# Kernel tuning notes

Hardware: AMD Instinct MI355X
Metric: run time of the kernel (lower is better)

The kernel has to match this reference:

```python
import jax, jax.numpy as jnp
import numpy as np


def _norm_group(pts, ref):
    # pts: [B,T,N,2], ref: [B,T,1,2]. Subtract reference point, divide both coords
    # by max(width,height) of the relative bbox (per frame), guarding scale==0.
    rel = pts - ref
    w = rel[..., 0].max(axis=-1) - rel[..., 0].min(axis=-1)
    h = rel[..., 1].max(axis=-1) - rel[..., 1].min(axis=-1)
    s = jnp.maximum(w, h)
    s = jnp.where(s == 0, jnp.ones_like(s), s)
    return rel / s[..., None, None]


def _prepare_input(x):
    B, T, _ = x.shape
    pts = x.reshape(B, T, 133, 2)
    left = _norm_group(pts[:, :, 91:112], pts[:, :, 9:10]).reshape(B, T, 42)
    right = _norm_group(pts[:, :, 112:133], pts[:, :, 10:11]).reshape(B, T, 42)
    center = pts[:, :, 0:1]
    left_arm = _norm_group(pts[:, :, (5, 7, 9), :], center).reshape(B, T, 6)
    right_arm = _norm_group(pts[:, :, (6, 8, 10), :], center).reshape(B, T, 6)
    return right, right_arm, left, left_arm


def _lstm(x, wih, whh, bih, bhh):
    # x: [B,T,F]; PyTorch gate order i,f,g,o. Returns all hidden states [B,T,H].
    B = x.shape[0]
    H = whh.shape[1]
    pre = jnp.einsum('btf,gf->btg', x, wih) + bih  # [B,T,4H]
    pre = pre.transpose(1, 0, 2)  # time-major for scan
    h0 = jnp.zeros((B, H), x.dtype)
    c0 = jnp.zeros((B, H), x.dtype)

    def step(carry, xt):
        h, c = carry
        g = xt + h @ whh.T + bhh
        i, f, gg, o = jnp.split(g, 4, axis=-1)
        i = jax.nn.sigmoid(i)
        f = jax.nn.sigmoid(f)
        gg = jnp.tanh(gg)
        o = jax.nn.sigmoid(o)
        c = f * c + i * gg
        h = o * jnp.tanh(c)
        return (h, c), h

    _, hs = jax.lax.scan(step, (h0, c0), pre)
    return hs.transpose(1, 0, 2)


def setup_inputs() -> dict:
    key = jax.random.key(0)
    ks = jax.random.split(key, 24)
    B, T = 128, 512
    NUM_CLASSES = 250
    HID = 2 * 64 + 2 * 32  # 192
    s = 0.1

    def p(k, shape):
        return jax.random.normal(k, shape, dtype=jnp.float32) * s

    inp = {'x': jax.random.normal(ks[0], (B, T, 266), dtype=jnp.float32)}
    # right hand LSTM: 42 -> 64
    inp['wih_rh'] = p(ks[1], (256, 42)); inp['whh_rh'] = p(ks[2], (256, 64))
    inp['bih_rh'] = p(ks[3], (256,));   inp['bhh_rh'] = p(ks[4], (256,))
    # right arm LSTM: 6 -> 32
    inp['wih_ra'] = p(ks[5], (128, 6));  inp['whh_ra'] = p(ks[6], (128, 32))
    inp['bih_ra'] = p(ks[7], (128,));   inp['bhh_ra'] = p(ks[8], (128,))
    # left hand LSTM: 42 -> 64
    inp['wih_lh'] = p(ks[9], (256, 42)); inp['whh_lh'] = p(ks[10], (256, 64))
    inp['bih_lh'] = p(ks[11], (256,));  inp['bhh_lh'] = p(ks[12], (256,))
    # left arm LSTM: 6 -> 32
    inp['wih_la'] = p(ks[13], (128, 6)); inp['whh_la'] = p(ks[14], (128, 32))
    inp['bih_la'] = p(ks[15], (128,));  inp['bhh_la'] = p(ks[16], (128,))
    # attention (Linear(192,1,bias=False)) and fc
    inp['att_w'] = p(ks[17], (1, HID))
    inp['fc_w'] = p(ks[18], (NUM_CLASSES, HID))
    inp['fc_b'] = p(ks[19], (NUM_CLASSES,))
    return inp


def reference(x, wih_rh, whh_rh, bih_rh, bhh_rh,
              wih_ra, whh_ra, bih_ra, bhh_ra,
              wih_lh, whh_lh, bih_lh, bhh_lh,
              wih_la, whh_la, bih_la, bhh_la,
              att_w, fc_w, fc_b):
    rh, ra, lh, la = _prepare_input(x)
    rh_out = _lstm(rh, wih_rh, whh_rh, bih_rh, bhh_rh)
    ra_out = _lstm(ra, wih_ra, whh_ra, bih_ra, bhh_ra)
    lh_out = _lstm(lh, wih_lh, whh_lh, bih_lh, bhh_lh)
    la_out = _lstm(la, wih_la, whh_la, bih_la, bhh_la)
    combined = jnp.concatenate([rh_out, ra_out, lh_out, la_out], axis=2)  # [B,T,192]
    scores = jnp.einsum('bth,oh->bto', combined, att_w)  # [B,T,1]
    weights = jax.nn.softmax(scores, axis=1)
    context = jnp.sum(weights * combined, axis=1)  # [B,192]
    out = context @ fc_w.T + fc_b  # [B,num_classes]
    return out, weights
```

## Files before the change

kernel.cpp:

```cpp
#include <hip/hip_runtime.h>
#include <math.h>

#define BATCH 128
#define TLEN 512
#define XF 266
#define HID 192
#define NC 250

typedef __attribute__((ext_vector_type(8))) short short8;
typedef __attribute__((ext_vector_type(4))) float float4v;

#define NL2E  -1.4426950408889634f
#define NL2E2 -2.8853900817779268f

__device__ __forceinline__ unsigned short f2bf(float f) {
  unsigned u = __float_as_uint(f);
  u += 0x7FFF + ((u >> 16) & 1);
  return (unsigned short)(u >> 16);
}
__device__ __forceinline__ float bf2f(unsigned short s) {
  return __uint_as_float(((unsigned)s) << 16);
}

__device__ __forceinline__ float exp2i(float x) {
#if __has_builtin(__builtin_amdgcn_exp2f)
  return __builtin_amdgcn_exp2f(x);
#else
  float r;
  asm("v_exp_f32 %0, %1" : "=v"(r) : "v"(x));
  return r;
#endif
}

__device__ __forceinline__ void lds_barrier() {
  asm volatile("s_waitcnt lgkmcnt(0)\n\ts_barrier" ::: "memory");
}


__device__ __forceinline__ void norm_hand(const float* __restrict__ xp,
                                          unsigned short* __restrict__ fp,
                                          int p0, int refp, int hs) {
  float rx = xp[2 * refp], ry = xp[2 * refp + 1];
  float px[21], py[21];
  float minx = 1e30f, maxx = -1e30f, miny = 1e30f, maxy = -1e30f;
#pragma unroll
  for (int i = 0; i < 21; ++i) {
    float ax = xp[2 * (p0 + i)] - rx;
    float ay = xp[2 * (p0 + i) + 1] - ry;
    px[i] = ax; py[i] = ay;
    minx = fminf(minx, ax); maxx = fmaxf(maxx, ax);
    miny = fminf(miny, ay); maxy = fmaxf(maxy, ay);
  }
  float s = fmaxf(maxx - minx, maxy - miny);
  if (s == 0.f) s = 1.f;
  float inv = 1.f / s;
#pragma unroll
  for (int i = 0; i < 21; ++i) {
    fp[2 * i] = f2bf(px[i] * inv);
    fp[2 * i + 1] = f2bf(py[i] * inv);
  }
  for (int i = 42; i < hs; ++i) fp[i] = 0;
}

__device__ __forceinline__ void norm_arm(const float* __restrict__ xp,
                                         unsigned short* __restrict__ fp,
                                         int a, int b, int c) {
  float rx = xp[0], ry = xp[1];
  float x0 = xp[2 * a] - rx, y0 = xp[2 * a + 1] - ry;
  float x1 = xp[2 * b] - rx, y1 = xp[2 * b + 1] - ry;
  float x2 = xp[2 * c] - rx, y2 = xp[2 * c + 1] - ry;
  float w = fmaxf(fmaxf(x0, x1), x2) - fminf(fminf(x0, x1), x2);
  float h = fmaxf(fmaxf(y0, y1), y2) - fminf(fminf(y0, y1), y2);
  float s = fmaxf(w, h);
  if (s == 0.f) s = 1.f;
  float inv = 1.f / s;
  fp[0] = f2bf(x0 * inv); fp[1] = f2bf(y0 * inv);
  fp[2] = f2bf(x1 * inv); fp[3] = f2bf(y1 * inv);
  fp[4] = f2bf(x2 * inv); fp[5] = f2bf(y2 * inv);
  fp[6] = 0; fp[7] = 0;
}

__global__ __launch_bounds__(256) void prep_kernel(
    const float* __restrict__ x,
    unsigned short* __restrict__ fHR, unsigned short* __restrict__ fHL,
    unsigned short* __restrict__ fAR, unsigned short* __restrict__ fAL,
    int mode) {
  int idx = blockIdx.x * 256 + threadIdx.x;
  if (idx >= BATCH * TLEN) return;
  int b = idx >> 9, t = idx & 511;
  const float* xp = x + (size_t)idx * XF;
  size_t hoff, aoff;
  int hs;
  if (mode) {
    hs = 64;
    int vh = b & 7;
    int rowh = (vh >> 1) * 4 + (vh & 1);
    hoff = (((size_t)(b >> 3) * TLEN + t) * 16 + rowh) * 64;
    int va = b & 15;
    int rowa = (va >> 3) * 16 + ((va & 7) >> 1) * 4 + (va & 1);
    aoff = (((size_t)(b >> 4) * TLEN + t) * 32 + rowa) * 8;
  } else {
    hs = 48;
    hoff = (((size_t)(b >> 4) * TLEN + t) * 16 + (b & 15)) * 48;
    aoff = (((size_t)(b >> 5) * TLEN + t) * 32 + (b & 31)) * 8;
  }
  norm_hand(xp, fHR + hoff, 112, 10, hs);
  norm_hand(xp, fHL + hoff, 91, 9, hs);
  norm_arm (xp, fAR + aoff, 6, 8, 10);
  norm_arm (xp, fAL + aoff, 5, 7, 9);
}


__global__ __launch_bounds__(256) void pack_kernel(
    const float* __restrict__ wi_rh, const float* __restrict__ wh_rh,
    const float* __restrict__ wi_ra, const float* __restrict__ wh_ra,
    const float* __restrict__ wi_lh, const float* __restrict__ wh_lh,
    const float* __restrict__ wi_la, const float* __restrict__ wh_la,
    unsigned short* __restrict__ btA_r, unsigned short* __restrict__ btA_l,
    unsigned short* __restrict__ btArm_r, unsigned short* __restrict__ btArm_l) {
  int blk = blockIdx.x, tid = threadIdx.x;
  if (blk < 2) {
    const float* wi = blk ? wi_lh : wi_rh;
    const float* wh = blk ? wh_lh : wh_rh;
    unsigned short* dst = blk ? btA_l : btA_r;
    for (int i = tid; i < 256 * 128; i += 256) {
      int g = i >> 7, k = i & 127;
      float s = ((g >> 6) == 2) ? NL2E2 : NL2E;
      float v = (k < 42) ? wi[g * 42 + k] : (k < 64 ? 0.f : wh[g * 64 + (k - 64)]);
      dst[i] = f2bf(v * s);
    }
  } else {
    const float* wi = (blk == 3) ? wi_la : wi_ra;
    const float* wh = (blk == 3) ? wh_la : wh_ra;
    unsigned short* dst = (blk == 3) ? btArm_l : btArm_r;
    for (int i = tid; i < 128 * 64; i += 256) {
      int g = i >> 6, k = i & 63;
      float s = ((g >> 5) == 2) ? NL2E2 : NL2E;
      float v = (k < 6) ? wi[g * 6 + k] : (k < 32 ? 0.f : wh[g * 32 + (k - 32)]);
      dst[i] = f2bf(v * s);
    }
  }
}


__global__ __launch_bounds__(256, 1) void pregemm_kernel(
    const unsigned short* __restrict__ f64R, const unsigned short* __restrict__ f64L,
    const float* __restrict__ wiR, const float* __restrict__ wiL,
    const float* __restrict__ biR, const float* __restrict__ bhR,
    const float* __restrict__ biL, const float* __restrict__ bhL,
    unsigned short* __restrict__ preR, unsigned short* __restrict__ preL) {
  int bx = blockIdx.x;
  int lr = bx >> 8, tile = (bx >> 4) & 15, tc = bx & 15;
  const unsigned short* f64 = lr ? f64L : f64R;
  const float* wi = lr ? wiL : wiR;
  const float* bi = lr ? biL : biR;
  const float* bh = lr ? bhL : bhR;
  unsigned short* pre = lr ? preL : preR;
  int tid = threadIdx.x, lane = tid & 63;
  int q = tid >> 6, n = lane & 15, quad = lane >> 4;
  float sq = (q == 2) ? NL2E2 : NL2E;

  short8 Vb[4][2];
  float bias[4];
#pragma unroll
  for (int jg = 0; jg < 4; ++jg) {
    int g = q * 64 + jg * 16 + n;
    bias[jg] = (bi[g] + bh[g]) * sq;
#pragma unroll
    for (int c = 0; c < 2; ++c) {
      short8 vb;
#pragma unroll
      for (int s = 0; s < 8; ++s) {
        int k = c * 32 + quad * 8 + s;
        vb[s] = (short)f2bf(k < 42 ? wi[g * 42 + k] * sq : 0.f);
      }
      Vb[jg][c] = vb;
    }
  }

  for (int i = 0; i < 32; ++i) {
    int t = tc * 32 + i;
    const unsigned short* ap = f64 + ((size_t)(tile * 512 + t) * 16 + n) * 64 + quad * 8;
    short8 Va0 = *(const short8*)ap;
    short8 Va1 = *(const short8*)(ap + 32);
    unsigned short* pb0 = pre + ((size_t)(tile * 2) * 512 + t) * 1024 + n * 16 + quad * 4 + q;
    unsigned short* pb1 = pb0 + (size_t)512 * 1024;
#pragma unroll
    for (int jg = 0; jg < 4; ++jg) {
      float4v acc = {bias[jg], bias[jg], bias[jg], bias[jg]};
      acc = __builtin_amdgcn_mfma_f32_16x16x32_bf16(Va0, Vb[jg][0], acc, 0, 0, 0);
      acc = __builtin_amdgcn_mfma_f32_16x16x32_bf16(Va1, Vb[jg][1], acc, 0, 0, 0);
      pb0[jg * 256] = f2bf(acc[0]);
      pb1[jg * 256] = f2bf(acc[1]);
    }
  }
}


template <int H, int CH, int STR, int MB, int SCH, int HOFF, bool HOIST, int RSEL>
__device__ __forceinline__ void lstm_core1(
    unsigned short* __restrict__ Ab0, unsigned short* __restrict__ Ab1,
    const float* __restrict__ wq,
    const float* __restrict__ wx,
    const float* __restrict__ bi, const float* __restrict__ bh,
    const unsigned short* __restrict__ featp,
    const unsigned short* __restrict__ prep_,
    unsigned short* __restrict__ combbase,
    int b0, int mrow0, int j0) {
  constexpr int XSH = MB * SCH * 8;
  int tid = threadIdx.x;
  int lane = tid & 63, n = lane & 15, quad = lane >> 4;

  short8 Vb[4][CH];
  float bias[4];
#pragma unroll
  for (int q = 0; q < 4; ++q) {
    float sq = (q == 2) ? NL2E2 : NL2E;
    int g = q * H + j0 + n;
    if (!HOIST) bias[q] = (bi[g] + bh[g]) * sq;
#pragma unroll
    for (int c = 0; c < CH; ++c) {
      short8 vb;
#pragma unroll
      for (int s = 0; s < 8; ++s) {
        int k = c * 32 + quad * 8 + s;
        float v;
        if (HOIST) {
          v = wq[(size_t)g * H + k];
        } else {
          v = (k < 6) ? wx[g * 6 + k]
                      : (k >= 32 ? wq[g * 32 + (k - 32)] : 0.f);
        }
        vb[s] = (short)f2bf(v * sq);
      }
      Vb[q][c] = vb;
    }
  }

  for (int i = tid; i < MB * STR; i += 256) { Ab0[i] = 0; Ab1[i] = 0; }
  __syncthreads();

  bool st = false;
  unsigned short *xd0 = nullptr, *xd1 = nullptr;
  const unsigned short* fp = nullptr;
  short8 xE, xO;
  if (!HOIST) {
    st = tid < MB * SCH;
    xd0 = Ab0 + tid * STR;
    xd1 = Ab1 + tid * STR;
    fp = featp + tid * 8;
    if (st) {
      *(short8*)xd0 = *(const short8*)fp;
      xO = *(const short8*)(fp + XSH);
      xE = *(const short8*)(fp + 2 * (size_t)XSH);
    }
    fp += 3 * (size_t)XSH;
  }

  const unsigned short *ppE = nullptr, *ppO = nullptr;
  uint2 pE = {0, 0}, pO = {0, 0};
  if (HOIST) {
    const unsigned short* pp0 = prep_ + (size_t)(j0 >> 4) * 256 + n * 16 + quad * 4;
    pE = *(const uint2*)pp0;
    pO = *(const uint2*)(pp0 + 1024);
    ppE = pp0 + 2 * 1024;
    ppO = pp0 + 3 * 1024;
  }

  float cc = 0.f;
  __syncthreads();

  const unsigned short* ard0 = Ab0 + (mrow0 + n) * STR;
  const unsigned short* ard1 = Ab1 + (mrow0 + n) * STR;
  unsigned short* hw0 = Ab0 + (mrow0 + quad * 4 + RSEL) * STR + HOFF + j0 + n;
  unsigned short* hw1 = Ab1 + (mrow0 + quad * 4 + RSEL) * STR + HOFF + j0 + n;
  unsigned short* cgp = combbase +
      ((size_t)(b0 + (mrow0 >> 1) + quad * 2) * TLEN) * HID + j0 + n;

  for (int tt = 0; tt < TLEN; tt += 2) {
    {
      const int t = tt;
      short8 Va[CH];
#pragma unroll
      for (int c = 0; c < CH; ++c)
        Va[c] = *(const short8*)(ard0 + c * 32 + quad * 8);

      float4v acc[4];
#pragma unroll
      for (int q = 0; q < 4; ++q) acc[q] = (float4v){0.f, 0.f, 0.f, 0.f};
      if (HOIST) {
        acc[0][RSEL] = __uint_as_float(pE.x << 16);
        acc[1][RSEL] = __uint_as_float(pE.x & 0xffff0000u);
        acc[2][RSEL] = __uint_as_float(pE.y << 16);
        acc[3][RSEL] = __uint_as_float(pE.y & 0xffff0000u);
        if (t + 2 < TLEN) pE = *(const uint2*)ppE;
        ppE += 2 * 1024;
      } else {
#pragma unroll
        for (int q = 0; q < 4; ++q) acc[q][RSEL] = bias[q];
      }
#pragma unroll
      for (int q = 0; q < 4; ++q)
#pragma unroll
        for (int c = 0; c < CH; ++c)
          acc[q] = __builtin_amdgcn_mfma_f32_16x16x32_bf16(Va[c], Vb[q][c], acc[q], 0, 0, 0);

      if (!HOIST) {
        if (st) {
          *(short8*)xd1 = xO;
          if (t + 3 < TLEN) xO = *(const short8*)fp;
        }
        fp += XSH;
      }

      float Ei = exp2i(acc[0][RSEL]);
      float Ef = exp2i(acc[1][RSEL]);
      float Eg = exp2i(acc[2][RSEL]);
      float Eo = exp2i(acc[3][RSEL]);
      float gf = __builtin_amdgcn_rcpf(1.f + Ef);
      float ig = (1.f - Eg) * __builtin_amdgcn_rcpf((1.f + Ei) * (1.f + Eg));
      float cv = fmaf(gf, cc, ig);
      cc = cv;
      float Ec = exp2i(cv * NL2E2);
      float hv = (1.f - Ec) * __builtin_amdgcn_rcpf((1.f + Eo) * (1.f + Ec));
      unsigned short hb = f2bf(hv);
      hw1[0] = hb;
      *cgp = hb;
      cgp += HID;
      lds_barrier();
    }
    {
      const int t = tt + 1;
      short8 Va[CH];
#pragma unroll
      for (int c = 0; c < CH; ++c)
        Va[c] = *(const short8*)(ard1 + c * 32 + quad * 8);

      float4v acc[4];
#pragma unroll
      for (int q = 0; q < 4; ++q) acc[q] = (float4v){0.f, 0.f, 0.f, 0.f};
      if (HOIST) {
        acc[0][RSEL] = __uint_as_float(pO.x << 16);
        acc[1][RSEL] = __uint_as_float(pO.x & 0xffff0000u);
        acc[2][RSEL] = __uint_as_float(pO.y << 16);
        acc[3][RSEL] = __uint_as_float(pO.y & 0xffff0000u);
        if (t + 2 < TLEN) pO = *(const uint2*)ppO;
        ppO += 2 * 1024;
      } else {
#pragma unroll
        for (int q = 0; q < 4; ++q) acc[q][RSEL] = bias[q];
      }
#pragma unroll
      for (int q = 0; q < 4; ++q)
#pragma unroll
        for (int c = 0; c < CH; ++c)
          acc[q] = __builtin_amdgcn_mfma_f32_16x16x32_bf16(Va[c], Vb[q][c], acc[q], 0, 0, 0);

      if (!HOIST) {
        if (st) {
          if (t + 1 < TLEN) *(short8*)xd0 = xE;
          if (t + 3 < TLEN) xE = *(const short8*)fp;
        }
        fp += XSH;
      }

      float Ei = exp2i(acc[0][RSEL]);
      float Ef = exp2i(acc[1][RSEL]);
      float Eg = exp2i(acc[2][RSEL]);
      float Eo = exp2i(acc[3][RSEL]);
      float gf = __builtin_amdgcn_rcpf(1.f + Ef);
      float ig = (1.f - Eg) * __builtin_amdgcn_rcpf((1.f + Ei) * (1.f + Eg));
      float cv = fmaf(gf, cc, ig);
      cc = cv;
      float Ec = exp2i(cv * NL2E2);
      float hv = (1.f - Ec) * __builtin_amdgcn_rcpf((1.f + Eo) * (1.f + Ec));
      unsigned short hb = f2bf(hv);
      hw0[0] = hb;
      *cgp = hb;
      cgp += HID;
      lds_barrier();
    }
  }
}

__global__ __launch_bounds__(256, 1) void lstm_hoist(
    const unsigned short* __restrict__ fAR, const unsigned short* __restrict__ fAL,
    const float* __restrict__ whh_rh, const float* __restrict__ whh_lh,
    const float* __restrict__ wih_ra, const float* __restrict__ whh_ra,
    const float* __restrict__ wih_la, const float* __restrict__ whh_la,
    const unsigned short* __restrict__ preR, const unsigned short* __restrict__ preL,
    const float* __restrict__ b1i, const float* __restrict__ b1h,
    const float* __restrict__ b3i, const float* __restrict__ b3h,
    unsigned short* __restrict__ combined) {
  __shared__ __align__(16) unsigned short A0[2304];
  __shared__ __align__(16) unsigned short A1[2304];
  int blk = blockIdx.x;
  int wave = threadIdx.x >> 6;
  if (blk < 64) {
    int lr = blk >> 5, rem = blk & 31, tl = rem >> 1, r = rem & 1;
    const unsigned short* pp = (lr ? preL : preR) + (size_t)rem * 512 * 1024;
    const float* wq = lr ? whh_lh : whh_rh;
    unsigned short* cmb = combined + (lr ? 96 : 0);
    if (r == 0)
      lstm_core1<64, 2, 72, 16, 0, 0, true, 0>(
          A0, A1, wq, nullptr, nullptr, nullptr, nullptr, pp, cmb,
          tl * 8 + 0, 0, wave * 16);
    else
      lstm_core1<64, 2, 72, 16, 0, 0, true, 1>(
          A0, A1, wq, nullptr, nullptr, nullptr, nullptr, pp, cmb,
          tl * 8 + 1, 0, wave * 16);
  } else {
    int a = blk - 64;
    int la = a >> 4, rem = a & 15, tl = rem >> 1, r = rem & 1;
    const unsigned short* fpz = (la ? fAL : fAR) + (size_t)tl * 512 * 256;
    const float* wxp = la ? wih_la : wih_ra;
    const float* wqp = la ? whh_la : whh_ra;
    const float* bip = la ? b3i : b1i;
    const float* bhp = la ? b3h : b1h;
    unsigned short* cmb = combined + (la ? 160 : 64);
    int mrow0 = (wave >> 1) * 16, j0 = (wave & 1) * 16;
    if (r == 0)
      lstm_core1<32, 2, 72, 32, 1, 32, false, 0>(
          A0, A1, wqp, wxp, bip, bhp, fpz, nullptr, cmb,
          tl * 16 + 0, mrow0, j0);
    else
      lstm_core1<32, 2, 72, 32, 1, 32, false, 1>(
          A0, A1, wqp, wxp, bip, bhp, fpz, nullptr, cmb,
          tl * 16 + 1, mrow0, j0);
  }
}


template <int H, int CH, int STR, int MB, int SCH, int HOFF, int RV>
__device__ __forceinline__ void lstm_core_fb(
    unsigned short* __restrict__ Ab0, unsigned short* __restrict__ Ab1,
    const unsigned short* __restrict__ Bt,
    const float* __restrict__ bi, const float* __restrict__ bh,
    const unsigned short* __restrict__ featp,
    unsigned short* __restrict__ combbase,
    int b0, int mrow0, int j0) {
  constexpr int K = CH * 32;
  constexpr int XSH = MB * SCH * 8;
  constexpr int JQ = H / 4;
  constexpr int VR = MB;
  int tid = threadIdx.x;
  int lane = tid & 63, n = lane & 15, quad = lane >> 4;

  short8 Vb[4][CH];
  float bias[4];
#pragma unroll
  for (int q = 0; q < 4; ++q) {
    int g = q * H + j0 + n;
    bias[q] = (bi[g] + bh[g]) * ((q == 2) ? NL2E2 : NL2E);
#pragma unroll
    for (int c = 0; c < CH; ++c)
      Vb[q][c] = *(const short8*)(Bt + (size_t)g * K + c * 32 + quad * 8);
  }

  for (int i = tid; i < MB * STR; i += 256) { Ab0[i] = 0; Ab1[i] = 0; }
  __syncthreads();

  bool st = tid < MB * SCH;
  int sm = SCH ? tid / SCH : 0, sc8 = SCH ? tid % SCH : 0;
  unsigned short* xd0 = Ab0 + sm * STR + sc8 * 8;
  unsigned short* xd1 = Ab1 + sm * STR + sc8 * 8;
  const unsigned short* fp = featp + tid * 8;
  short8 xE, xO;
  if (st) {
    *(short8*)xd0 = *(const short8*)fp;
    xO = *(const short8*)(fp + XSH);
    xE = *(const short8*)(fp + 2 * (size_t)XSH);
  }
  fp += 3 * (size_t)XSH;

  float4v cc = {0.f, 0.f, 0.f, 0.f};
  __syncthreads();

  const unsigned short* ard0 = Ab0 + (mrow0 + n) * STR;
  const unsigned short* ard1 = Ab1 + (mrow0 + n) * STR;
  unsigned short* hw0 = Ab0 + (mrow0 + quad * 4) * STR + HOFF + j0 + n;
  unsigned short* hw1 = Ab1 + (mrow0 + quad * 4) * STR + HOFF + j0 + n;

  int vi = tid / JQ, fjq = tid % JQ;
  bool fon = tid < VR * JQ;
  int fm = vi;
  const unsigned short* fl0 = Ab0 + fm * STR + HOFF + fjq * 4;
  const unsigned short* fl1 = Ab1 + fm * STR + HOFF + fjq * 4;
  unsigned short* cfp = combbase + ((size_t)(b0 + vi) * TLEN) * HID + fjq * 4;

#define ACT_FB(hw)                                                            \
  _Pragma("unroll")                                                           \
  for (int r = 0; r < RV; ++r) {                                              \
    float Ei = exp2i(acc[0][r]);                                              \
    float Ef = exp2i(acc[1][r]);                                              \
    float Eg = exp2i(acc[2][r]);                                              \
    float Eo = exp2i(acc[3][r]);                                              \
    float gf = __builtin_amdgcn_rcpf(1.f + Ef);                               \
    float ig = (1.f - Eg) * __builtin_amdgcn_rcpf((1.f + Ei) * (1.f + Eg));   \
    float cv = fmaf(gf, cc[r], ig);                                           \
    cc[r] = cv;                                                               \
    float Ec = exp2i(cv * NL2E2);                                             \
    float hv = (1.f - Ec) * __builtin_amdgcn_rcpf((1.f + Eo) * (1.f + Ec));   \
    (hw)[r * STR] = f2bf(hv);                                                 \
  }

  for (int tt = 0; tt < TLEN; tt += 2) {
    {
      const int t = tt;
      if (fon && t > 0) {
        *(uint2*)cfp = *(const uint2*)fl0;
        cfp += HID;
      }
      short8 Va[CH];
#pragma unroll
      for (int c = 0; c < CH; ++c)
        Va[c] = *(const short8*)(ard0 + c * 32 + quad * 8);
      float4v acc[4];
#pragma unroll
      for (int q = 0; q < 4; ++q)
        acc[q] = (float4v){bias[q], bias[q], bias[q], bias[q]};
#pragma unroll
      for (int q = 0; q < 4; ++q)
#pragma unroll
        for (int c = 0; c < CH; ++c)
          acc[q] = __builtin_amdgcn_mfma_f32_16x16x32_bf16(Va[c], Vb[q][c], acc[q], 0, 0, 0);
      if (st) {
        *(short8*)xd1 = xO;
        if (t + 3 < TLEN) xO = *(const short8*)fp;
      }
      fp += XSH;
      ACT_FB(hw1)
      lds_barrier();
    }
    {
      const int t = tt + 1;
      if (fon) {
        *(uint2*)cfp = *(const uint2*)fl1;
        cfp += HID;
      }
      short8 Va[CH];
#pragma unroll
      for (int c = 0; c < CH; ++c)
        Va[c] = *(const short8*)(ard1 + c * 32 + quad * 8);
      float4v acc[4];
#pragma unroll
      for (int q = 0; q < 4; ++q)
        acc[q] = (float4v){bias[q], bias[q], bias[q], bias[q]};
#pragma unroll
      for (int q = 0; q < 4; ++q)
#pragma unroll
        for (int c = 0; c < CH; ++c)
          acc[q] = __builtin_amdgcn_mfma_f32_16x16x32_bf16(Va[c], Vb[q][c], acc[q], 0, 0, 0);
      if (st) {
        if (t + 1 < TLEN) *(short8*)xd0 = xE;
        if (t + 3 < TLEN) xE = *(const short8*)fp;
      }
      fp += XSH;
      ACT_FB(hw0)
      lds_barrier();
    }
  }
  if (fon) *(uint2*)cfp = *(const uint2*)fl0;
#undef ACT_FB
}

__global__ __launch_bounds__(256, 1) void lstm_fb(
    const unsigned short* __restrict__ fHR, const unsigned short* __restrict__ fHL,
    const unsigned short* __restrict__ fAR, const unsigned short* __restrict__ fAL,
    const unsigned short* __restrict__ btA_r, const unsigned short* __restrict__ btA_l,
    const unsigned short* __restrict__ btArm_r, const unsigned short* __restrict__ btArm_l,
    const float* __restrict__ b0i, const float* __restrict__ b0h,
    const float* __restrict__ b1i, const float* __restrict__ b1h,
    const float* __restrict__ b2i, const float* __restrict__ b2h,
    const float* __restrict__ b3i, const float* __restrict__ b3h,
    unsigned short* __restrict__ combined) {
  __shared__ __align__(16) unsigned short A0[2304];
  __shared__ __align__(16) unsigned short A1[2304];
  int blk = blockIdx.x;
  int wave = threadIdx.x >> 6;
  if (blk < 16) {
    int lr = blk >> 3, tl = blk & 7;
    lstm_core_fb<64, 4, 136, 16, 6, 64, 4>(
        A0, A1, lr ? btA_l : btA_r, lr ? b2i : b0i, lr ? b2h : b0h,
        (lr ? fHL : fHR) + (size_t)tl * 512 * 768,
        combined + (lr ? 96 : 0), tl * 16, 0, wave * 16);
  } else {
    int a = blk - 16;
    int la = a >> 2, tl = a & 3;
    lstm_core_fb<32, 2, 72, 32, 1, 32, 4>(
        A0, A1, la ? btArm_l : btArm_r, la ? b3i : b1i, la ? b3h : b1h,
        (la ? fAL : fAR) + (size_t)tl * 512 * 256,
        combined + (la ? 160 : 64), tl * 32, (wave >> 1) * 16, (wave & 1) * 16);
  }
}


__global__ __launch_bounds__(512) void attn_kernel(const unsigned short* __restrict__ combined,
                                                   const float* __restrict__ att_w,
                                                   const float* __restrict__ fc_w,
                                                   const float* __restrict__ fc_b,
                                                   float* __restrict__ dout) {
  __shared__ float sc[TLEN];
  __shared__ float aw[HID];
  __shared__ float pctx[8][HID];
  __shared__ float ctx[HID];
  __shared__ float red[8];
  int b = blockIdx.x, tid = threadIdx.x;
  int lane = tid & 63, wave = tid >> 6;
  const unsigned short* cb = combined + (size_t)b * TLEN * HID;
  if (tid < HID) aw[tid] = att_w[tid];
  __syncthreads();
  float a0 = aw[lane], a1 = aw[lane + 64], a2 = aw[lane + 128];

  int t0 = wave * 64;
  for (int t = t0; t < t0 + 64; t += 2) {
    const unsigned short* r0 = cb + (size_t)t * HID;
    const unsigned short* r1 = r0 + HID;
    float p0 = a0 * bf2f(r0[lane]) + a1 * bf2f(r0[lane + 64]) + a2 * bf2f(r0[lane + 128]);
    float p1 = a0 * bf2f(r1[lane]) + a1 * bf2f(r1[lane + 64]) + a2 * bf2f(r1[lane + 128]);
#pragma unroll
    for (int o = 32; o; o >>= 1) {
      p0 += __shfl_xor(p0, o, 64);
      p1 += __shfl_xor(p1, o, 64);
    }
    if (lane == 0) { sc[t] = p0; sc[t + 1] = p1; }
  }
  __syncthreads();

  float e = sc[tid];
  float lmax = e;
#pragma unroll
  for (int o = 32; o; o >>= 1) lmax = fmaxf(lmax, __shfl_xor(lmax, o, 64));
  if (lane == 0) red[wave] = lmax;
  __syncthreads();
  float m = red[0];
#pragma unroll
  for (int w = 1; w < 8; ++w) m = fmaxf(m, red[w]);
  __syncthreads();
  float ex = __expf(e - m);
  float ls = ex;
#pragma unroll
  for (int o = 32; o; o >>= 1) ls += __shfl_xor(ls, o, 64);
  if (lane == 0) red[wave] = ls;
  __syncthreads();
  float S = red[0];
#pragma unroll
  for (int w = 1; w < 8; ++w) S += red[w];
  float wgt = ex / S;
  sc[tid] = wgt;
  dout[BATCH * NC + b * TLEN + tid] = wgt;
  __syncthreads();

#pragma unroll
  for (int p = 0; p < 3; ++p) {
    int h = p * 64 + lane;
    float c0 = 0.f, c1 = 0.f, c2 = 0.f, c3 = 0.f;
    for (int t = t0; t < t0 + 64; t += 4) {
      c0 += sc[t] * bf2f(cb[(size_t)t * HID + h]);
      c1 += sc[t + 1] * bf2f(cb[(size_t)(t + 1) * HID + h]);
      c2 += sc[t + 2] * bf2f(cb[(size_t)(t + 2) * HID + h]);
      c3 += sc[t + 3] * bf2f(cb[(size_t)(t + 3) * HID + h]);
    }
    pctx[wave][h] = (c0 + c1) + (c2 + c3);
  }
  __syncthreads();
  if (tid < HID) {
    float s = pctx[0][tid];
#pragma unroll
    for (int w = 1; w < 8; ++w) s += pctx[w][tid];
    ctx[tid] = s;
  }
  __syncthreads();

  if (tid < NC) {
    const float* wr = fc_w + (size_t)tid * HID;
    float s0 = fc_b[tid], s1 = 0.f, s2 = 0.f, s3 = 0.f;
#pragma unroll
    for (int h = 0; h < HID; h += 4) {
      s0 += ctx[h] * wr[h];
      s1 += ctx[h + 1] * wr[h + 1];
      s2 += ctx[h + 2] * wr[h + 2];
      s3 += ctx[h + 3] * wr[h + 3];
    }
    dout[b * NC + tid] = (s0 + s1) + (s2 + s3);
  }
}


extern "C" void kernel_launch(void* const* d_in, const int* in_sizes, int n_in,
                              void* d_out, int out_size, void* d_ws, size_t ws_size,
                              hipStream_t stream) {
  const float* x = (const float*)d_in[0];
  const float* wih_rh = (const float*)d_in[1];
  const float* whh_rh = (const float*)d_in[2];
  const float* bih_rh = (const float*)d_in[3];
  const float* bhh_rh = (const float*)d_in[4];
  const float* wih_ra = (const float*)d_in[5];
  const float* whh_ra = (const float*)d_in[6];
  const float* bih_ra = (const float*)d_in[7];
  const float* bhh_ra = (const float*)d_in[8];
  const float* wih_lh = (const float*)d_in[9];
  const float* whh_lh = (const float*)d_in[10];
  const float* bih_lh = (const float*)d_in[11];
  const float* bhh_lh = (const float*)d_in[12];
  const float* wih_la = (const float*)d_in[13];
  const float* whh_la = (const float*)d_in[14];
  const float* bih_la = (const float*)d_in[15];
  const float* bhh_la = (const float*)d_in[16];
  const float* att_w = (const float*)d_in[17];
  const float* fc_w = (const float*)d_in[18];
  const float* fc_b = (const float*)d_in[19];

  const size_t SZ_COMB   = (size_t)BATCH * TLEN * HID * 2;
  const size_t SZ_FARM_H = (size_t)8 * TLEN * 32 * 8 * 2;
  const size_t SZ_FARM_F = (size_t)4 * TLEN * 32 * 8 * 2;
  const size_t SZ_F64    = (size_t)16 * TLEN * 16 * 64 * 2;
  const size_t SZ_F48    = (size_t)8 * TLEN * 16 * 48 * 2;
  const size_t SZ_PRE    = (size_t)32 * TLEN * 1024 * 2;
  const size_t NEED_FULL = SZ_COMB + 2 * SZ_FARM_H + 2 * SZ_F64 + 2 * SZ_PRE;
  bool hoist = ws_size >= NEED_FULL;

  char* p = (char*)d_ws;
  unsigned short* combined = (unsigned short*)p; p += SZ_COMB;
  unsigned short *fAR, *fAL;
  unsigned short *fHR, *fHL, *preR = nullptr, *preL = nullptr;
  unsigned short *btA_r = nullptr, *btA_l = nullptr, *btArm_r = nullptr, *btArm_l = nullptr;
  if (hoist) {
    fAR = (unsigned short*)p; p += SZ_FARM_H;
    fAL = (unsigned short*)p; p += SZ_FARM_H;
    fHR = (unsigned short*)p; p += SZ_F64;
    fHL = (unsigned short*)p; p += SZ_F64;
    preR = (unsigned short*)p; p += SZ_PRE;
    preL = (unsigned short*)p; p += SZ_PRE;
  } else {
    fAR = (unsigned short*)p; p += SZ_FARM_F;
    fAL = (unsigned short*)p; p += SZ_FARM_F;
    fHR = (unsigned short*)p; p += SZ_F48;
    fHL = (unsigned short*)p; p += SZ_F48;
    btA_r = (unsigned short*)p; p += 65536;
    btA_l = (unsigned short*)p; p += 65536;
    btArm_r = (unsigned short*)p; p += 16384;
    btArm_l = (unsigned short*)p;
  }

  prep_kernel<<<dim3((BATCH * TLEN + 255) / 256), 256, 0, stream>>>(
      x, fHR, fHL, fAR, fAL, hoist ? 1 : 0);
  if (hoist) {
    pregemm_kernel<<<dim3(512), 256, 0, stream>>>(
        fHR, fHL, wih_rh, wih_lh, bih_rh, bhh_rh, bih_lh, bhh_lh, preR, preL);
    lstm_hoist<<<dim3(96), 256, 0, stream>>>(
        fAR, fAL, whh_rh, whh_lh, wih_ra, whh_ra, wih_la, whh_la,
        preR, preL, bih_ra, bhh_ra, bih_la, bhh_la, combined);
  } else {
    pack_kernel<<<dim3(4), 256, 0, stream>>>(
        wih_rh, whh_rh, wih_ra, whh_ra, wih_lh, whh_lh, wih_la, whh_la,
        btA_r, btA_l, btArm_r, btArm_l);
    lstm_fb<<<dim3(24), 256, 0, stream>>>(
        fHR, fHL, fAR, fAL, btA_r, btA_l, btArm_r, btArm_l,
        bih_rh, bhh_rh, bih_ra, bhh_ra, bih_lh, bhh_lh, bih_la, bhh_la, combined);
  }
  attn_kernel<<<dim3(BATCH), 512, 0, stream>>>(combined, att_w, fc_w, fc_b, (float*)d_out);
}
```

Baseline: 430.3 us.

## Pack hand features densely and restructure pregemm to store all four gates per row

The hand feature buffer now uses a dense 16-row tile per batch group instead of the padded 8-of-16 interleaved layout, halving its size and the pregemm work. Pregemm assigns one wave per 16-column gate group, computes all four gates for 16 rows and writes them as packed uint2 stores across four row-select planes, with software prefetch of the next timestep's inputs. The hand LSTM now splits each tile into four instances using RSEL 0..3 with a new batch-stride template parameter. The intent is to remove wasted padded MFMA rows and scattered 2-byte stores in the precompute stage, at the cost of changed indexing that must stay consistent between producer and consumer.

Result: faster. 387.5 us (-9.9%).

```diff
diff --git a/kernel.cpp b/kernel.cpp
--- a/kernel.cpp
+++ b/kernel.cpp
@@ -93,9 +93,7 @@
   int hs;
   if (mode) {
     hs = 64;
-    int vh = b & 7;
-    int rowh = (vh >> 1) * 4 + (vh & 1);
-    hoff = (((size_t)(b >> 3) * TLEN + t) * 16 + rowh) * 64;
+    hoff = (((size_t)(b >> 4) * TLEN + t) * 16 + (b & 15)) * 64;
     int va = b & 15;
     int rowa = (va >> 3) * 16 + ((va & 7) >> 1) * 4 + (va & 1);
     aoff = (((size_t)(b >> 4) * TLEN + t) * 32 + rowa) * 8;
@@ -150,22 +148,22 @@
     const float* __restrict__ biL, const float* __restrict__ bhL,
     unsigned short* __restrict__ preR, unsigned short* __restrict__ preL) {
   int bx = blockIdx.x;
-  int lr = bx >> 8, tile = (bx >> 4) & 15, tc = bx & 15;
+  int lr = bx >> 7, tile = (bx >> 4) & 7, tc = bx & 15;
   const unsigned short* f64 = lr ? f64L : f64R;
   const float* wi = lr ? wiL : wiR;
   const float* bi = lr ? biL : biR;
   const float* bh = lr ? bhL : bhR;
   unsigned short* pre = lr ? preL : preR;
   int tid = threadIdx.x, lane = tid & 63;
-  int q = tid >> 6, n = lane & 15, quad = lane >> 4;
-  float sq = (q == 2) ? NL2E2 : NL2E;
+  int jg = tid >> 6, n = lane & 15, quad = lane >> 4;
 
   short8 Vb[4][2];
   float bias[4];
 #pragma unroll
-  for (int jg = 0; jg < 4; ++jg) {
+  for (int q = 0; q < 4; ++q) {
+    float sq = (q == 2) ? NL2E2 : NL2E;
     int g = q * 64 + jg * 16 + n;
-    bias[jg] = (bi[g] + bh[g]) * sq;
+    bias[q] = (bi[g] + bh[g]) * sq;
 #pragma unroll
     for (int c = 0; c < 2; ++c) {
       short8 vb;
@@ -174,30 +172,46 @@
         int k = c * 32 + quad * 8 + s;
         vb[s] = (short)f2bf(k < 42 ? wi[g * 42 + k] * sq : 0.f);
       }
-      Vb[jg][c] = vb;
-    }
-  }
-
+      Vb[q][c] = vb;
+    }
+  }
+
+  const unsigned short* ap =
+      f64 + ((size_t)(tile * 512 + tc * 32) * 16 + n) * 64 + quad * 8;
+  short8 VaC0 = *(const short8*)ap;
+  short8 VaC1 = *(const short8*)(ap + 32);
+  ap += 1024;
+  unsigned short* pb = pre + ((size_t)(tile * 4) * 512 + tc * 32) * 1024 +
+                       jg * 256 + quad * 64 + n * 4;
   for (int i = 0; i < 32; ++i) {
-    int t = tc * 32 + i;
-    const unsigned short* ap = f64 + ((size_t)(tile * 512 + t) * 16 + n) * 64 + quad * 8;
-    short8 Va0 = *(const short8*)ap;
-    short8 Va1 = *(const short8*)(ap + 32);
-    unsigned short* pb0 = pre + ((size_t)(tile * 2) * 512 + t) * 1024 + n * 16 + quad * 4 + q;
-    unsigned short* pb1 = pb0 + (size_t)512 * 1024;
-#pragma unroll
-    for (int jg = 0; jg < 4; ++jg) {
-      float4v acc = {bias[jg], bias[jg], bias[jg], bias[jg]};
-      acc = __builtin_amdgcn_mfma_f32_16x16x32_bf16(Va0, Vb[jg][0], acc, 0, 0, 0);
-      acc = __builtin_amdgcn_mfma_f32_16x16x32_bf16(Va1, Vb[jg][1], acc, 0, 0, 0);
-      pb0[jg * 256] = f2bf(acc[0]);
-      pb1[jg * 256] = f2bf(acc[1]);
-    }
-  }
-}
-
-
-template <int H, int CH, int STR, int MB, int SCH, int HOFF, bool HOIST, int RSEL>
+    short8 VaN0, VaN1;
+    if (i + 1 < 32) {
+      VaN0 = *(const short8*)ap;
+      VaN1 = *(const short8*)(ap + 32);
+    }
+    ap += 1024;
+    float4v acc[4];
+#pragma unroll
+    for (int q = 0; q < 4; ++q) {
+      acc[q] = (float4v){bias[q], bias[q], bias[q], bias[q]};
+      acc[q] = __builtin_amdgcn_mfma_f32_16x16x32_bf16(VaC0, Vb[q][0], acc[q], 0, 0, 0);
+      acc[q] = __builtin_amdgcn_mfma_f32_16x16x32_bf16(VaC1, Vb[q][1], acc[q], 0, 0, 0);
+    }
+#pragma unroll
+    for (int r = 0; r < 4; ++r) {
+      uint2 u;
+      u.x = (unsigned)f2bf(acc[0][r]) | ((unsigned)f2bf(acc[1][r]) << 16);
+      u.y = (unsigned)f2bf(acc[2][r]) | ((unsigned)f2bf(acc[3][r]) << 16);
+      *(uint2*)(pb + (size_t)r * (512 * 1024)) = u;
+    }
+    pb += 1024;
+    VaC0 = VaN0;
+    VaC1 = VaN1;
+  }
+}
+
+
+template <int H, int CH, int STR, int MB, int SCH, int HOFF, bool HOIST, int RSEL, int BQS>
 __device__ __forceinline__ void lstm_core1(
     unsigned short* __restrict__ Ab0, unsigned short* __restrict__ Ab1,
     const float* __restrict__ wq,
@@ -260,7 +274,7 @@
   const unsigned short *ppE = nullptr, *ppO = nullptr;
   uint2 pE = {0, 0}, pO = {0, 0};
   if (HOIST) {
-    const unsigned short* pp0 = prep_ + (size_t)(j0 >> 4) * 256 + n * 16 + quad * 4;
+    const unsigned short* pp0 = prep_ + (size_t)(j0 >> 4) * 256 + quad * 64 + n * 4;
     pE = *(const uint2*)pp0;
     pO = *(const uint2*)(pp0 + 1024);
     ppE = pp0 + 2 * 1024;
@@ -275,7 +289,7 @@
   unsigned short* hw0 = Ab0 + (mrow0 + quad * 4 + RSEL) * STR + HOFF + j0 + n;
   unsigned short* hw1 = Ab1 + (mrow0 + quad * 4 + RSEL) * STR + HOFF + j0 + n;
   unsigned short* cgp = combbase +
-      ((size_t)(b0 + (mrow0 >> 1) + quad * 2) * TLEN) * HID + j0 + n;
+      ((size_t)(b0 + (mrow0 >> 1) + quad * BQS) * TLEN) * HID + j0 + n;
 
   for (int tt = 0; tt < TLEN; tt += 2) {
     {
@@ -397,18 +411,23 @@
   int blk = blockIdx.x;
   int wave = threadIdx.x >> 6;
   if (blk < 64) {
-    int lr = blk >> 5, rem = blk & 31, tl = rem >> 1, r = rem & 1;
-    const unsigned short* pp = (lr ? preL : preR) + (size_t)rem * 512 * 1024;
+    int lr = blk >> 5, inst = blk & 31, tile = inst >> 2, r = inst & 3;
+    const unsigned short* pp = (lr ? preL : preR) + (size_t)inst * 512 * 1024;
     const float* wq = lr ? whh_lh : whh_rh;
     unsigned short* cmb = combined + (lr ? 96 : 0);
+    int b0 = tile * 16 + r;
     if (r == 0)
-      lstm_core1<64, 2, 72, 16, 0, 0, true, 0>(
-          A0, A1, wq, nullptr, nullptr, nullptr, nullptr, pp, cmb,
-          tl * 8 + 0, 0, wave * 16);
+      lstm_core1<64, 2, 72, 16, 0, 0, true, 0, 4>(
+          A0, A1, wq, nullptr, nullptr, nullptr, nullptr, pp, cmb, b0, 0, wave * 16);
+    else if (r == 1)
+      lstm_core1<64, 2, 72, 16, 0, 0, true, 1, 4>(
+          A0, A1, wq, nullptr, nullptr, nullptr, nullptr, pp, cmb, b0, 0, wave * 16);
+    else if (r == 2)
+      lstm_core1<64, 2, 72, 16, 0, 0, true, 2, 4>(
+          A0, A1, wq, nullptr, nullptr, nullptr, nullptr, pp, cmb, b0, 0, wave * 16);
     else
-      lstm_core1<64, 2, 72, 16, 0, 0, true, 1>(
-          A0, A1, wq, nullptr, nullptr, nullptr, nullptr, pp, cmb,
-          tl * 8 + 1, 0, wave * 16);
+      lstm_core1<64, 2, 72, 16, 0, 0, true, 3, 4>(
+          A0, A1, wq, nullptr, nullptr, nullptr, nullptr, pp, cmb, b0, 0, wave * 16);
   } else {
     int a = blk - 64;
     int la = a >> 4, rem = a & 15, tl = rem >> 1, r = rem & 1;
@@ -420,11 +439,11 @@
     unsigned short* cmb = combined + (la ? 160 : 64);
     int mrow0 = (wave >> 1) * 16, j0 = (wave & 1) * 16;
     if (r == 0)
-      lstm_core1<32, 2, 72, 32, 1, 32, false, 0>(
+      lstm_core1<32, 2, 72, 32, 1, 32, false, 0, 2>(
           A0, A1, wqp, wxp, bip, bhp, fpz, nullptr, cmb,
           tl * 16 + 0, mrow0, j0);
     else
-      lstm_core1<32, 2, 72, 32, 1, 32, false, 1>(
+      lstm_core1<32, 2, 72, 32, 1, 32, false, 1, 2>(
           A0, A1, wqp, wxp, bip, bhp, fpz, nullptr, cmb,
           tl * 16 + 1, mrow0, j0);
   }
@@ -714,7 +733,7 @@
   const size_t SZ_COMB   = (size_t)BATCH * TLEN * HID * 2;
   const size_t SZ_FARM_H = (size_t)8 * TLEN * 32 * 8 * 2;
   const size_t SZ_FARM_F = (size_t)4 * TLEN * 32 * 8 * 2;
-  const size_t SZ_F64    = (size_t)16 * TLEN * 16 * 64 * 2;
+  const size_t SZ_F64    = (size_t)8 * TLEN * 16 * 64 * 2;
   const size_t SZ_F48    = (size_t)8 * TLEN * 16 * 48 * 2;
   const size_t SZ_PRE    = (size_t)32 * TLEN * 1024 * 2;
   const size_t NEED_FULL = SZ_COMB + 2 * SZ_FARM_H + 2 * SZ_F64 + 2 * SZ_PRE;
@@ -746,7 +765,7 @@
   prep_kernel<<<dim3((BATCH * TLEN + 255) / 256), 256, 0, stream>>>(
       x, fHR, fHL, fAR, fAL, hoist ? 1 : 0);
   if (hoist) {
-    pregemm_kernel<<<dim3(512), 256, 0, stream>>>(
+    pregemm_kernel<<<dim3(256), 256, 0, stream>>>(
         fHR, fHL, wih_rh, wih_lh, bih_rh, bhh_rh, bih_lh, bhh_lh, preR, preL);
     lstm_hoist<<<dim3(96), 256, 0, stream>>>(
         fAR, fAL, whh_rh, whh_lh, wih_ra, whh_ra, wih_la, whh_la,
```
